# Kernel tuning notes

Measured on AMD Instinct MI355X. Metric: run time of the kernel, lower is better.

The kernel has to match this reference:

```python
import jax, jax.numpy as jnp
import numpy as np


def setup_inputs() -> dict:
    key = jax.random.key(0)
    k1, k2, k3, k4 = jax.random.split(key, 4)
    B, T, C, H = 8, 2048, 1024, 64
    x = jax.random.normal(k1, (B, T, C), dtype=jnp.float32)
    # nn.Linear weights, stored as (in, out) for x @ W
    Wk = jax.random.normal(k2, (C, H), dtype=jnp.float32) * (C ** -0.5)
    Wq = jax.random.normal(k3, (C, H), dtype=jnp.float32) * (C ** -0.5)
    Wv = jax.random.normal(k4, (C, H), dtype=jnp.float32) * (C ** -0.5)
    return {"x": x, "Wk": Wk, "Wq": Wq, "Wv": Wv}


def reference(x, Wk, Wq, Wv):
    B, T, C = x.shape
    k = x @ Wk  # [B,T,H]
    q = x @ Wq  # [B,T,H]
    v = x @ Wv  # [B,T,H]
    # NOTE: original scales by C**-0.5 (full embed dim), not head_size**-0.5
    wei = jnp.einsum("bth,bsh->bts", q, k) * (C ** -0.5)  # [B,T,T]
    causal = jnp.tril(jnp.ones((T, T), dtype=bool))
    wei = jnp.where(causal, wei, -jnp.inf)
    wei = jax.nn.softmax(wei, axis=-1)
    # dropout is identity in eval/reference mode
    out = jnp.einsum("bts,bsh->bth", wei, v)  # [B,T,H]
    return out
```

## Files before the change

kernel.cpp:

```cpp
#include <hip/hip_runtime.h>
#include <hip/hip_bf16.h>
#include <math.h>

#define B_ 8
#define T_ 2048
#define C_ 1024
#define H_ 64
#define M_ (B_*T_)
#define BMQ 32

typedef __attribute__((ext_vector_type(8))) short short8;
typedef __attribute__((ext_vector_type(4))) float f32x4;
typedef unsigned int u32;

__device__ __forceinline__ unsigned short f2bf(float f) {
    u32 u = __builtin_bit_cast(u32, f);
    u += 0x7FFFu + ((u >> 16) & 1u);
    return (unsigned short)(u >> 16);
}

__device__ __forceinline__ void gl2lds16(const void* g, void* l) {
    __builtin_amdgcn_global_load_lds(
        (const __attribute__((address_space(1))) u32*)g,
        (__attribute__((address_space(3))) u32*)l, 16, 0, 0);
}

__global__ __launch_bounds__(256) void wconv(
    const float* __restrict__ Wk, const float* __restrict__ Wq,
    const float* __restrict__ Wv, unsigned short* __restrict__ wb)
{
    int idx = blockIdx.x * 256 + threadIdx.x;
    int n = idx % 192, k = idx / 192;
    const float* src = (n < 64) ? Wk : (n < 128 ? Wq : Wv);
    float sc = (n >= 64 && n < 128) ? 0.03125f : 1.0f;
    float v = src[(size_t)k * H_ + (n & 63)] * sc;
    int k2 = k * 2;
    int dst = (k2 & ~127) | ((k2 & 127) ^ ((n & 7) << 4));
    *(unsigned short*)((char*)wb + (size_t)n * 2048 + dst) = f2bf(v);
}

__global__ __launch_bounds__(256) void qkv_mm(
    const float* __restrict__ x, const unsigned short* __restrict__ wb,
    unsigned short* __restrict__ kb, unsigned short* __restrict__ qb,
    unsigned short* __restrict__ vT)
{
    __shared__ __align__(16) unsigned short Xs[32][72];
    __shared__ __align__(16) unsigned short Ws[2][192 * 64];

    const int tid = threadIdx.x;
    const int wid = tid >> 6;
    const int lane = tid & 63;
    const int lr = lane & 15;
    const int lg = lane >> 4;
    const int m0 = blockIdx.x * BMQ;

    const int xrow = tid >> 3;
    const int xcol = (tid & 7) * 8;
    const float* xbase = x + (size_t)(m0 + xrow) * C_ + xcol;

    f32x4 acc[2][3];
    for (int r = 0; r < 2; ++r)
        for (int c = 0; c < 3; ++c)
            acc[r][c] = (f32x4){0.f, 0.f, 0.f, 0.f};

    float4 xr0 = *reinterpret_cast<const float4*>(xbase);
    float4 xr1 = *reinterpret_cast<const float4*>(xbase + 4);
    {
        for (int p = 0; p < 6; ++p) {
            int c = p * 256 + tid;
            int n = c >> 3, c16 = c & 7;
            gl2lds16((const char*)wb + (size_t)n * 2048 + c16 * 16,
                     (char*)&Ws[0][0] + c * 16);
        }
    }

    for (int t = 0; t < 16; ++t) {
        __syncthreads();
        short8 xw;
        xw[0] = (short)f2bf(xr0.x); xw[1] = (short)f2bf(xr0.y);
        xw[2] = (short)f2bf(xr0.z); xw[3] = (short)f2bf(xr0.w);
        xw[4] = (short)f2bf(xr1.x); xw[5] = (short)f2bf(xr1.y);
        xw[6] = (short)f2bf(xr1.z); xw[7] = (short)f2bf(xr1.w);
        *reinterpret_cast<short8*>(&Xs[xrow][xcol]) = xw;
        __syncthreads();

        if (t < 15) {
            xr0 = *reinterpret_cast<const float4*>(xbase + (t + 1) * 64);
            xr1 = *reinterpret_cast<const float4*>(xbase + (t + 1) * 64 + 4);
            int buf = (t + 1) & 1;
            for (int p = 0; p < 6; ++p) {
                int c = p * 256 + tid;
                int n = c >> 3, c16 = c & 7;
                gl2lds16((const char*)wb + (size_t)n * 2048 + (t + 1) * 128 + c16 * 16,
                         (char*)&Ws[buf][0] + c * 16);
            }
        }

        const char* wbuf = (const char*)&Ws[t & 1][0];
        for (int kc = 0; kc < 2; ++kc) {
            short8 af[2], bfr[3];
            for (int rt = 0; rt < 2; ++rt)
                af[rt] = *reinterpret_cast<const short8*>(&Xs[rt * 16 + lr][kc * 32 + lg * 8]);
            for (int ct = 0; ct < 3; ++ct) {
                int n = (wid * 3 + ct) * 16 + lr;
                int cb = (kc * 64 + lg * 16) ^ ((n & 7) << 4);
                bfr[ct] = *reinterpret_cast<const short8*>(wbuf + n * 128 + cb);
            }
            for (int rt = 0; rt < 2; ++rt)
                for (int ct = 0; ct < 3; ++ct)
                    acc[rt][ct] = __builtin_amdgcn_mfma_f32_16x16x32_bf16(
                        af[rt], bfr[ct], acc[rt][ct], 0, 0, 0);
        }
    }

    for (int rt = 0; rt < 2; ++rt) {
        for (int ct = 0; ct < 3; ++ct) {
            int n = (wid * 3 + ct) * 16 + lr;
            int col = n & 63;
            for (int i = 0; i < 4; ++i) {
                int m = m0 + rt * 16 + lg * 4 + i;
                unsigned short val = f2bf(acc[rt][ct][i]);
                if (n < 64)       kb[(size_t)m * H_ + col] = val;
                else if (n < 128) qb[(size_t)m * H_ + col] = val;
                else              vT[(size_t)(m >> 11) * (64 * T_) + (size_t)col * T_ + (m & (T_ - 1))] = val;
            }
        }
    }
}

__global__ __launch_bounds__(64) void attn2(
    const unsigned short* __restrict__ kb,
    const unsigned short* __restrict__ qb,
    const unsigned short* __restrict__ vT,
    float* __restrict__ out)
{
    __shared__ __align__(16) unsigned short Ps[16][72];

    const int lane = threadIdx.x;
    const int lr = lane & 15;
    const int lg = lane >> 4;
    const int b = blockIdx.y;
    const int bx = blockIdx.x;
    const size_t base = (size_t)b * T_ * H_;
    const unsigned short* vTb = vT + (size_t)b * 64 * T_;

    for (int ph = 0; ph < 2; ++ph) {
        const int tile = ph ? (127 - bx) : bx;
        const int q0w = tile * 16;

        short8 qf[2];
        for (int kc = 0; kc < 2; ++kc)
            qf[kc] = *reinterpret_cast<const short8*>(
                qb + base + (size_t)(q0w + lr) * H_ + kc * 32 + lg * 8);

        f32x4 o[4];
        float mrun[4], lrun[4];
        for (int dt = 0; dt < 4; ++dt) o[dt] = (f32x4){0.f, 0.f, 0.f, 0.f};
        for (int i = 0; i < 4; ++i) { mrun[i] = -INFINITY; lrun[i] = 0.f; }

        for (int kv0 = 0; kv0 <= q0w; kv0 += 64) {
            f32x4 s[4];
            for (int kt = 0; kt < 4; ++kt) s[kt] = (f32x4){0.f, 0.f, 0.f, 0.f};
            for (int kc = 0; kc < 2; ++kc) {
                for (int kt = 0; kt < 4; ++kt) {
                    short8 kf = *reinterpret_cast<const short8*>(
                        kb + base + (size_t)(kv0 + kt * 16 + lr) * H_ + kc * 32 + lg * 8);
                    s[kt] = __builtin_amdgcn_mfma_f32_16x16x32_bf16(qf[kc], kf, s[kt], 0, 0, 0);
                }
            }

            for (int i = 0; i < 4; ++i) {
                int row = q0w + lg * 4 + i;
                float sv[4];
                float mx = -INFINITY;
                for (int kt = 0; kt < 4; ++kt) {
                    int key = kv0 + kt * 16 + lr;
                    float v = (key <= row) ? s[kt][i] : -INFINITY;
                    sv[kt] = v;
                    mx = fmaxf(mx, v);
                }
                for (int d = 8; d; d >>= 1) mx = fmaxf(mx, __shfl_xor(mx, d));
                float mn  = fmaxf(mrun[i], mx);
                float fac = __expf(mrun[i] - mn);
                float rs  = 0.f;
                for (int kt = 0; kt < 4; ++kt) {
                    float p = __expf(sv[kt] - mn);
                    rs += p;
                    Ps[lg * 4 + i][kt * 16 + lr] = f2bf(p);
                }
                for (int d = 8; d; d >>= 1) rs += __shfl_xor(rs, d);
                lrun[i] = lrun[i] * fac + rs;
                mrun[i] = mn;
                for (int dt = 0; dt < 4; ++dt)
                    o[dt][i] *= fac;
            }

            for (int kc = 0; kc < 2; ++kc) {
                short8 pf = *reinterpret_cast<const short8*>(&Ps[lr][kc * 32 + lg * 8]);
                for (int dt = 0; dt < 4; ++dt) {
                    short8 vf = *reinterpret_cast<const short8*>(
                        vTb + (size_t)(dt * 16 + lr) * T_ + kv0 + kc * 32 + lg * 8);
                    o[dt] = __builtin_amdgcn_mfma_f32_16x16x32_bf16(pf, vf, o[dt], 0, 0, 0);
                }
            }
        }

        for (int i = 0; i < 4; ++i) {
            float inv = 1.0f / lrun[i];
            int row = q0w + lg * 4 + i;
            for (int dt = 0; dt < 4; ++dt)
                out[base + (size_t)row * H_ + dt * 16 + lr] = o[dt][i] * inv;
        }
    }
}

extern "C" void kernel_launch(void* const* d_in, const int* in_sizes, int n_in,
                              void* d_out, int out_size, void* d_ws, size_t ws_size,
                              hipStream_t stream) {
    const float* x  = (const float*)d_in[0];
    const float* Wk = (const float*)d_in[1];
    const float* Wq = (const float*)d_in[2];
    const float* Wv = (const float*)d_in[3];
    float* out = (float*)d_out;

    unsigned short* kb = (unsigned short*)d_ws;
    unsigned short* qb = kb + (size_t)M_ * H_;
    unsigned short* vT = qb + (size_t)M_ * H_;
    unsigned short* wb = vT + (size_t)M_ * H_;

    wconv<<<768, 256, 0, stream>>>(Wk, Wq, Wv, wb);
    qkv_mm<<<M_ / BMQ, 256, 0, stream>>>(x, wb, kb, qb, vT);
    attn2<<<dim3(64, B_), 64, 0, stream>>>(kb, qb, vT, out);
}
```

Baseline: 187.5 us.

## Split attention KV range across four waves and simplify QKV projection without LDS

```diff
diff --git a/kernel.cpp b/kernel.cpp
--- a/kernel.cpp
+++ b/kernel.cpp
@@ -7,7 +7,6 @@
 #define C_ 1024
 #define H_ 64
 #define M_ (B_*T_)
-#define BMQ 32
 
 typedef __attribute__((ext_vector_type(8))) short short8;
 typedef __attribute__((ext_vector_type(4))) float f32x4;
@@ -19,24 +18,18 @@
     return (unsigned short)(u >> 16);
 }
 
-__device__ __forceinline__ void gl2lds16(const void* g, void* l) {
-    __builtin_amdgcn_global_load_lds(
-        (const __attribute__((address_space(1))) u32*)g,
-        (__attribute__((address_space(3))) u32*)l, 16, 0, 0);
-}
-
 __global__ __launch_bounds__(256) void wconv(
     const float* __restrict__ Wk, const float* __restrict__ Wq,
     const float* __restrict__ Wv, unsigned short* __restrict__ wb)
 {
-    int idx = blockIdx.x * 256 + threadIdx.x;
-    int n = idx % 192, k = idx / 192;
+    int n = blockIdx.x;
     const float* src = (n < 64) ? Wk : (n < 128 ? Wq : Wv);
     float sc = (n >= 64 && n < 128) ? 0.03125f : 1.0f;
-    float v = src[(size_t)k * H_ + (n & 63)] * sc;
-    int k2 = k * 2;
-    int dst = (k2 & ~127) | ((k2 & 127) ^ ((n & 7) << 4));
-    *(unsigned short*)((char*)wb + (size_t)n * 2048 + dst) = f2bf(v);
+    int col = n & 63;
+    for (int c = 0; c < 4; ++c) {
+        int k = c * 256 + threadIdx.x;
+        wb[(size_t)n * C_ + k] = f2bf(src[(size_t)k * H_ + col] * sc);
+    }
 }
 
 __global__ __launch_bounds__(256) void qkv_mm(
@@ -44,173 +37,161 @@
     unsigned short* __restrict__ kb, unsigned short* __restrict__ qb,
     unsigned short* __restrict__ vT)
 {
-    __shared__ __align__(16) unsigned short Xs[32][72];
-    __shared__ __align__(16) unsigned short Ws[2][192 * 64];
-
     const int tid = threadIdx.x;
     const int wid = tid >> 6;
     const int lane = tid & 63;
     const int lr = lane & 15;
     const int lg = lane >> 4;
-    const int m0 = blockIdx.x * BMQ;
-
-    const int xrow = tid >> 3;
-    const int xcol = (tid & 7) * 8;
-    const float* xbase = x + (size_t)(m0 + xrow) * C_ + xcol;
-
-    f32x4 acc[2][3];
-    for (int r = 0; r < 2; ++r)
-        for (int c = 0; c < 3; ++c)
-            acc[r][c] = (f32x4){0.f, 0.f, 0.f, 0.f};
-
-    float4 xr0 = *reinterpret_cast<const float4*>(xbase);
-    float4 xr1 = *reinterpret_cast<const float4*>(xbase + 4);
-    {
-        for (int p = 0; p < 6; ++p) {
-            int c = p * 256 + tid;
-            int n = c >> 3, c16 = c & 7;
-            gl2lds16((const char*)wb + (size_t)n * 2048 + c16 * 16,
-                     (char*)&Ws[0][0] + c * 16);
-        }
-    }
-
-    for (int t = 0; t < 16; ++t) {
-        __syncthreads();
-        short8 xw;
-        xw[0] = (short)f2bf(xr0.x); xw[1] = (short)f2bf(xr0.y);
-        xw[2] = (short)f2bf(xr0.z); xw[3] = (short)f2bf(xr0.w);
-        xw[4] = (short)f2bf(xr1.x); xw[5] = (short)f2bf(xr1.y);
-        xw[6] = (short)f2bf(xr1.z); xw[7] = (short)f2bf(xr1.w);
-        *reinterpret_cast<short8*>(&Xs[xrow][xcol]) = xw;
-        __syncthreads();
-
-        if (t < 15) {
-            xr0 = *reinterpret_cast<const float4*>(xbase + (t + 1) * 64);
-            xr1 = *reinterpret_cast<const float4*>(xbase + (t + 1) * 64 + 4);
-            int buf = (t + 1) & 1;
-            for (int p = 0; p < 6; ++p) {
-                int c = p * 256 + tid;
-                int n = c >> 3, c16 = c & 7;
-                gl2lds16((const char*)wb + (size_t)n * 2048 + (t + 1) * 128 + c16 * 16,
-                         (char*)&Ws[buf][0] + c * 16);
-            }
-        }
-
-        const char* wbuf = (const char*)&Ws[t & 1][0];
-        for (int kc = 0; kc < 2; ++kc) {
-            short8 af[2], bfr[3];
-            for (int rt = 0; rt < 2; ++rt)
-                af[rt] = *reinterpret_cast<const short8*>(&Xs[rt * 16 + lr][kc * 32 + lg * 8]);
-            for (int ct = 0; ct < 3; ++ct) {
-                int n = (wid * 3 + ct) * 16 + lr;
-                int cb = (kc * 64 + lg * 16) ^ ((n & 7) << 4);
-                bfr[ct] = *reinterpret_cast<const short8*>(wbuf + n * 128 + cb);
-            }
-            for (int rt = 0; rt < 2; ++rt)
-                for (int ct = 0; ct < 3; ++ct)
-                    acc[rt][ct] = __builtin_amdgcn_mfma_f32_16x16x32_bf16(
-                        af[rt], bfr[ct], acc[rt][ct], 0, 0, 0);
-        }
-    }
-
-    for (int rt = 0; rt < 2; ++rt) {
-        for (int ct = 0; ct < 3; ++ct) {
-            int n = (wid * 3 + ct) * 16 + lr;
-            int col = n & 63;
-            for (int i = 0; i < 4; ++i) {
-                int m = m0 + rt * 16 + lg * 4 + i;
-                unsigned short val = f2bf(acc[rt][ct][i]);
-                if (n < 64)       kb[(size_t)m * H_ + col] = val;
-                else if (n < 128) qb[(size_t)m * H_ + col] = val;
-                else              vT[(size_t)(m >> 11) * (64 * T_) + (size_t)col * T_ + (m & (T_ - 1))] = val;
-            }
-        }
-    }
-}
-
-__global__ __launch_bounds__(64) void attn2(
+    const int m0 = blockIdx.x * 16;
+
+    const float* xrow = x + (size_t)(m0 + lr) * C_ + lg * 8;
+    const unsigned short* wrow0 = wb + (size_t)(wid * 48 +  0 + lr) * C_ + lg * 8;
+    const unsigned short* wrow1 = wb + (size_t)(wid * 48 + 16 + lr) * C_ + lg * 8;
+    const unsigned short* wrow2 = wb + (size_t)(wid * 48 + 32 + lr) * C_ + lg * 8;
+
+    f32x4 acc[3];
+    for (int c = 0; c < 3; ++c) acc[c] = (f32x4){0.f, 0.f, 0.f, 0.f};
+
+    #pragma unroll 4
+    for (int t = 0; t < 32; ++t) {
+        int off = t * 32;
+        float4 a0 = *reinterpret_cast<const float4*>(xrow + off);
+        float4 a1 = *reinterpret_cast<const float4*>(xrow + off + 4);
+        short8 af;
+        af[0] = (short)f2bf(a0.x); af[1] = (short)f2bf(a0.y);
+        af[2] = (short)f2bf(a0.z); af[3] = (short)f2bf(a0.w);
+        af[4] = (short)f2bf(a1.x); af[5] = (short)f2bf(a1.y);
+        af[6] = (short)f2bf(a1.z); af[7] = (short)f2bf(a1.w);
+        short8 b0 = *reinterpret_cast<const short8*>(wrow0 + off);
+        short8 b1 = *reinterpret_cast<const short8*>(wrow1 + off);
+        short8 b2 = *reinterpret_cast<const short8*>(wrow2 + off);
+        acc[0] = __builtin_amdgcn_mfma_f32_16x16x32_bf16(af, b0, acc[0], 0, 0, 0);
+        acc[1] = __builtin_amdgcn_mfma_f32_16x16x32_bf16(af, b1, acc[1], 0, 0, 0);
+        acc[2] = __builtin_amdgcn_mfma_f32_16x16x32_bf16(af, b2, acc[2], 0, 0, 0);
+    }
+
+    for (int ct = 0; ct < 3; ++ct) {
+        int n = wid * 48 + ct * 16 + lr;
+        int col = n & 63;
+        for (int i = 0; i < 4; ++i) {
+            int m = m0 + lg * 4 + i;
+            unsigned short val = f2bf(acc[ct][i]);
+            if (n < 64)       kb[(size_t)m * H_ + col] = val;
+            else if (n < 128) qb[(size_t)m * H_ + col] = val;
+            else              vT[((size_t)(m >> 11) * H_ + col) * T_ + (m & (T_ - 1))] = val;
+        }
+    }
+}
+
+__global__ __launch_bounds__(256) void attn3(
     const unsigned short* __restrict__ kb,
     const unsigned short* __restrict__ qb,
     const unsigned short* __restrict__ vT,
     float* __restrict__ out)
 {
-    __shared__ __align__(16) unsigned short Ps[16][72];
-
-    const int lane = threadIdx.x;
-    const int lr = lane & 15;
-    const int lg = lane >> 4;
-    const int b = blockIdx.y;
-    const int bx = blockIdx.x;
+    __shared__ __align__(16) unsigned short Ps[4][16][72];
+    __shared__ float Om[4][16][64];
+    __shared__ float Mv[4][16], Lv[4][16], Fac[4][16], InvL[16];
+
+    const int tid  = threadIdx.x;
+    const int wid  = tid >> 6;
+    const int lane = tid & 63;
+    const int lr   = lane & 15;
+    const int lg   = lane >> 4;
+    const int b    = blockIdx.y;
+    const int bx   = blockIdx.x;
+    const int tile = (bx & 1) ? (127 - (bx >> 1)) : (bx >> 1);
+    const int q0   = tile * 16;
+    const int nsteps = (tile >> 2) + 1;
     const size_t base = (size_t)b * T_ * H_;
-    const unsigned short* vTb = vT + (size_t)b * 64 * T_;
-
-    for (int ph = 0; ph < 2; ++ph) {
-        const int tile = ph ? (127 - bx) : bx;
-        const int q0w = tile * 16;
-
-        short8 qf[2];
-        for (int kc = 0; kc < 2; ++kc)
-            qf[kc] = *reinterpret_cast<const short8*>(
-                qb + base + (size_t)(q0w + lr) * H_ + kc * 32 + lg * 8);
-
-        f32x4 o[4];
-        float mrun[4], lrun[4];
-        for (int dt = 0; dt < 4; ++dt) o[dt] = (f32x4){0.f, 0.f, 0.f, 0.f};
-        for (int i = 0; i < 4; ++i) { mrun[i] = -INFINITY; lrun[i] = 0.f; }
-
-        for (int kv0 = 0; kv0 <= q0w; kv0 += 64) {
-            f32x4 s[4];
-            for (int kt = 0; kt < 4; ++kt) s[kt] = (f32x4){0.f, 0.f, 0.f, 0.f};
-            for (int kc = 0; kc < 2; ++kc) {
-                for (int kt = 0; kt < 4; ++kt) {
-                    short8 kf = *reinterpret_cast<const short8*>(
-                        kb + base + (size_t)(kv0 + kt * 16 + lr) * H_ + kc * 32 + lg * 8);
-                    s[kt] = __builtin_amdgcn_mfma_f32_16x16x32_bf16(qf[kc], kf, s[kt], 0, 0, 0);
-                }
-            }
-
-            for (int i = 0; i < 4; ++i) {
-                int row = q0w + lg * 4 + i;
-                float sv[4];
-                float mx = -INFINITY;
-                for (int kt = 0; kt < 4; ++kt) {
-                    int key = kv0 + kt * 16 + lr;
-                    float v = (key <= row) ? s[kt][i] : -INFINITY;
-                    sv[kt] = v;
-                    mx = fmaxf(mx, v);
-                }
-                for (int d = 8; d; d >>= 1) mx = fmaxf(mx, __shfl_xor(mx, d));
-                float mn  = fmaxf(mrun[i], mx);
-                float fac = __expf(mrun[i] - mn);
-                float rs  = 0.f;
-                for (int kt = 0; kt < 4; ++kt) {
-                    float p = __expf(sv[kt] - mn);
-                    rs += p;
-                    Ps[lg * 4 + i][kt * 16 + lr] = f2bf(p);
-                }
-                for (int d = 8; d; d >>= 1) rs += __shfl_xor(rs, d);
-                lrun[i] = lrun[i] * fac + rs;
-                mrun[i] = mn;
-                for (int dt = 0; dt < 4; ++dt)
-                    o[dt][i] *= fac;
-            }
-
-            for (int kc = 0; kc < 2; ++kc) {
-                short8 pf = *reinterpret_cast<const short8*>(&Ps[lr][kc * 32 + lg * 8]);
-                for (int dt = 0; dt < 4; ++dt) {
-                    short8 vf = *reinterpret_cast<const short8*>(
-                        vTb + (size_t)(dt * 16 + lr) * T_ + kv0 + kc * 32 + lg * 8);
-                    o[dt] = __builtin_amdgcn_mfma_f32_16x16x32_bf16(pf, vf, o[dt], 0, 0, 0);
-                }
+    const unsigned short* vTb = vT + (size_t)b * H_ * T_;
+
+    short8 qf[2];
+    for (int kc = 0; kc < 2; ++kc)
+        qf[kc] = *reinterpret_cast<const short8*>(
+            qb + base + (size_t)(q0 + lr) * H_ + kc * 32 + lg * 8);
+
+    f32x4 o[4];
+    float mrun[4], lrun[4];
+    for (int dt = 0; dt < 4; ++dt) o[dt] = (f32x4){0.f, 0.f, 0.f, 0.f};
+    for (int i = 0; i < 4; ++i) { mrun[i] = -INFINITY; lrun[i] = 0.f; }
+
+    for (int s = wid; s < nsteps; s += 4) {
+        const int kv0 = s * 64;
+
+        f32x4 sv4[4];
+        for (int kt = 0; kt < 4; ++kt) sv4[kt] = (f32x4){0.f, 0.f, 0.f, 0.f};
+        for (int kc = 0; kc < 2; ++kc) {
+            for (int kt = 0; kt < 4; ++kt) {
+                short8 kf = *reinterpret_cast<const short8*>(
+                    kb + base + (size_t)(kv0 + kt * 16 + lr) * H_ + kc * 32 + lg * 8);
+                sv4[kt] = __builtin_amdgcn_mfma_f32_16x16x32_bf16(qf[kc], kf, sv4[kt], 0, 0, 0);
             }
         }
 
         for (int i = 0; i < 4; ++i) {
-            float inv = 1.0f / lrun[i];
-            int row = q0w + lg * 4 + i;
+            int row = q0 + lg * 4 + i;
+            float sv[4];
+            float mx = -INFINITY;
+            for (int kt = 0; kt < 4; ++kt) {
+                int key = kv0 + kt * 16 + lr;
+                float v = (key <= row) ? sv4[kt][i] : -INFINITY;
+                sv[kt] = v;
+                mx = fmaxf(mx, v);
+            }
+            for (int d = 8; d; d >>= 1) mx = fmaxf(mx, __shfl_xor(mx, d));
+            float mn  = fmaxf(mrun[i], mx);
+            float fac = __expf(mrun[i] - mn);
+            float rs  = 0.f;
+            for (int kt = 0; kt < 4; ++kt) {
+                float p = __expf(sv[kt] - mn);
+                rs += p;
+                Ps[wid][lg * 4 + i][kt * 16 + lr] = f2bf(p);
+            }
+            for (int d = 8; d; d >>= 1) rs += __shfl_xor(rs, d);
+            lrun[i] = lrun[i] * fac + rs;
+            mrun[i] = mn;
             for (int dt = 0; dt < 4; ++dt)
-                out[base + (size_t)row * H_ + dt * 16 + lr] = o[dt][i] * inv;
-        }
+                o[dt][i] *= fac;
+        }
+
+        for (int kc = 0; kc < 2; ++kc) {
+            short8 pf = *reinterpret_cast<const short8*>(&Ps[wid][lr][kc * 32 + lg * 8]);
+            for (int dt = 0; dt < 4; ++dt) {
+                short8 vf = *reinterpret_cast<const short8*>(
+                    vTb + (size_t)(dt * 16 + lr) * T_ + kv0 + kc * 32 + lg * 8);
+                o[dt] = __builtin_amdgcn_mfma_f32_16x16x32_bf16(pf, vf, o[dt], 0, 0, 0);
+            }
+        }
+    }
+
+    for (int dt = 0; dt < 4; ++dt)
+        for (int i = 0; i < 4; ++i)
+            Om[wid][lg * 4 + i][dt * 16 + lr] = o[dt][i];
+    if (lr == 0)
+        for (int i = 0; i < 4; ++i) {
+            Mv[wid][lg * 4 + i] = mrun[i];
+            Lv[wid][lg * 4 + i] = lrun[i];
+        }
+    __syncthreads();
+    if (tid < 16) {
+        float M = Mv[0][tid];
+        for (int w = 1; w < 4; ++w) M = fmaxf(M, Mv[w][tid]);
+        float L = 0.f;
+        for (int w = 0; w < 4; ++w) {
+            float f = __expf(Mv[w][tid] - M);
+            Fac[w][tid] = f;
+            L += Lv[w][tid] * f;
+        }
+        InvL[tid] = 1.0f / L;
+    }
+    __syncthreads();
+    for (int e = 0; e < 4; ++e) {
+        int idx = e * 256 + tid;
+        int row = idx >> 6, d = idx & 63;
+        float v = 0.f;
+        for (int w = 0; w < 4; ++w) v += Om[w][row][d] * Fac[w][row];
+        out[base + (size_t)(q0 + row) * H_ + d] = v * InvL[row];
     }
 }
 
@@ -228,7 +209,7 @@
     unsigned short* vT = qb + (size_t)M_ * H_;
     unsigned short* wb = vT + (size_t)M_ * H_;
 
-    wconv<<<768, 256, 0, stream>>>(Wk, Wq, Wv, wb);
-    qkv_mm<<<M_ / BMQ, 256, 0, stream>>>(x, wb, kb, qb, vT);
-    attn2<<<dim3(64, B_), 64, 0, stream>>>(kb, qb, vT, out);
-}
+    wconv<<<192, 256, 0, stream>>>(Wk, Wq, Wv, wb);
+    qkv_mm<<<M_ / 16, 256, 0, stream>>>(x, wb, kb, qb, vT);
+    attn3<<<dim3(128, B_), 256, 0, stream>>>(kb, qb, vT, out);
+}
```

Result: slower. 222.1 us (+18.4%).
